# Kernel tuning notes

Hardware: AMD Instinct MI355X
Metric: run time of the kernel (lower is better)

Reference implementation:

```python
import math
import jax, jax.numpy as jnp
import numpy as np
from jax import lax

CELL = 8
BINS = 9


def setup_inputs() -> dict:
    key = jax.random.key(0)
    x = jax.random.uniform(key, (64, 3, 224, 224), dtype=jnp.float32)
    return {"x": x}


def reference(x):
    N, C, H, W = x.shape
    # Fixed Sobel buffers: one output channel summing over all input channels.
    sob = jnp.array([[-1.0, 0.0, 1.0], [-2.0, 0.0, 2.0], [-1.0, 0.0, 1.0]], dtype=x.dtype)
    kx = jnp.broadcast_to(sob, (1, C, 3, 3))          # SobelX weight [O=1, I=C, 3, 3]
    ky = jnp.broadcast_to(sob.T, (1, C, 3, 3))        # SobelY weight
    dn = ('NCHW', 'OIHW', 'NCHW')
    gx = lax.conv_general_dilated(x, kx, (1, 1), 'SAME', dimension_numbers=dn)  # [N,1,H,W]
    gy = lax.conv_general_dilated(x, ky, (1, 1), 'SAME', dimension_numbers=dn)
    mag = jnp.sqrt(gx * gx + gy * gy)                 # [N,1,H,W]
    ang = jnp.abs(jnp.arctan2(gx, gy))                # unsigned gradients -> [0, pi]
    bin_idx = jnp.floor(ang / math.pi * (BINS - 1)).astype(jnp.int32)  # [N,1,H,W], values in [0, BINS-1]
    # scatter_(1, bin_idx, mag) == one-hot along bin axis times magnitude
    onehot = (bin_idx == jnp.arange(BINS, dtype=jnp.int32)[None, :, None, None]).astype(x.dtype)  # [N,BINS,H,W]
    vol = onehot * mag                                # broadcast over bin axis
    # AvgPool2d(cell) * cell^2 == per-cell sum
    hog = vol.reshape(N, BINS, H // CELL, CELL, W // CELL, CELL).sum(axis=(3, 5))  # [N,BINS,H/8,W/8]
    return hog.reshape(N, -1)
```

## Files before the change

### kernel.cpp

```cpp
#include <hip/hip_runtime.h>
#include <math.h>


namespace {
constexpr int Himg = 224;
constexpr int Wimg = 224;
constexpr int NCELL = 28;
constexpr int BINS  = 9;
constexpr int ROWS  = 18;
constexpr int LDSW  = 232;
constexpr int NCHUNK = ROWS * 56;

__global__ __launch_bounds__(512) void hog_kernel(const float* __restrict__ x,
                                                  float* __restrict__ out) {
    const int n  = blockIdx.y;
    const int pr = blockIdx.x;
    const int t  = threadIdx.x;

    __shared__ float s[ROWS][LDSW];
    __shared__ float h2[448 * BINS];

    if (t < ROWS * 8) {
        int r = t >> 3;
        int c = t & 7;
        int col = (c < 4) ? c : (224 + c);
        s[r][col] = 0.0f;
    }

    const int h0 = pr * 16 - 1;
    const float* xb = x + (size_t)n * 3 * Himg * Wimg;

    float4 va[2];
    int    lofs[2];
    bool   act[2];
#pragma unroll
    for (int k = 0; k < 2; ++k) {
        int idx = t + 512 * k;
        bool pred = idx < NCHUNK;
        int r = pred ? (idx / 56) : 0;
        int q = idx - r * 56;
        int w = q * 4;
        int h = h0 + r;
        act[k]  = pred;
        lofs[k] = r * LDSW + 4 + w;
        float4 v = make_float4(0.f, 0.f, 0.f, 0.f);
        if (pred && h >= 0 && h < Himg) {
            const float* r0 = xb + (size_t)h * Wimg + w;
            float4 a = *(const float4*)(r0);
            float4 b = *(const float4*)(r0 + Himg * Wimg);
            float4 c4 = *(const float4*)(r0 + 2 * Himg * Wimg);
            v.x = a.x + b.x + c4.x;
            v.y = a.y + b.y + c4.y;
            v.z = a.z + b.z + c4.z;
            v.w = a.w + b.w + c4.w;
        }
        va[k] = v;
    }
#pragma unroll
    for (int k = 0; k < 2; ++k)
        if (act[k]) *(float4*)&((float*)s)[lofs[k]] = va[k];
    __syncthreads();

    const float PI_F = 3.14159265358979323846f;
    const float CK[8] = {0.92387953f, 0.70710678f, 0.38268343f, 0.0f,
                         -0.38268343f, -0.70710678f, -0.92387953f, -1.0f};

    if (t < 448) {
        const int g = t >> 5 >= 7 ? 1 : 0;
        const int gg = t / 224;
        const int w  = t - gg * 224;
        (void)g;
        const int rb = gg * 8;
        float ml = s[rb][3 + w], mc = s[rb][4 + w], mr = s[rb][5 + w];
        float zl = s[rb + 1][3 + w], zc = s[rb + 1][4 + w], zr = s[rb + 1][5 + w];
        float acc[BINS];
#pragma unroll
        for (int j = 0; j < BINS; ++j) acc[j] = 0.0f;

#pragma unroll
        for (int i = 0; i < 8; ++i) {
            float pl = s[rb + i + 2][3 + w];
            float pc = s[rb + i + 2][4 + w];
            float pr2 = s[rb + i + 2][5 + w];

            float gx = (mr - ml) + 2.0f * (zr - zl) + (pr2 - pl);
            float gy = (pl + 2.0f * pc + pr2) - (ml + 2.0f * mc + mr);
            float mag = sqrtf(gx * gx + gy * gy);

            float negy = -gy;
            int bin = 0;
            float guard = 1e30f;
#pragma unroll
            for (int j = 0; j < 8; ++j) {
                float sj = fmaf(mag, CK[j], negy);
                bin += (sj >= 0.0f) ? 1 : 0;
                guard = fminf(guard, fabsf(sj));
            }
            if (guard < mag * 1e-4f) {
                float ang = fabsf(atan2f(gx, gy));
                bin = (int)(ang / PI_F * 8.0f);
                bin = bin > 8 ? 8 : bin;
            }
#pragma unroll
            for (int j = 0; j < BINS; ++j) acc[j] += (bin == j) ? mag : 0.0f;

            ml = zl; mc = zc; mr = zr;
            zl = pl; zc = pc; zr = pr2;
        }
#pragma unroll
        for (int j = 0; j < BINS; ++j) h2[t * BINS + j] = acc[j];
    }
    __syncthreads();

    if (t < 2 * NCELL * BINS) {
        int grp = t / (NCELL * BINS);
        int rem = t - grp * (NCELL * BINS);
        int bin = rem / NCELL;
        int cw  = rem - bin * NCELL;
        int cr  = pr * 2 + grp;
        float v = 0.0f;
#pragma unroll
        for (int c = 0; c < 8; ++c)
            v += h2[(grp * 224 + cw * 8 + c) * BINS + bin];
        out[((size_t)n * BINS + bin) * (NCELL * NCELL) + (size_t)cr * NCELL + cw] = v;
    }
}
}

extern "C" void kernel_launch(void* const* d_in, const int* in_sizes, int n_in,
                              void* d_out, int out_size, void* d_ws, size_t ws_size,
                              hipStream_t stream) {
    const float* x = (const float*)d_in[0];
    float* out = (float*)d_out;
    const int N = in_sizes[0] / (3 * Himg * Wimg);
    dim3 grid(NCELL / 2, N);
    hog_kernel<<<grid, 512, 0, stream>>>(x, out);
}
```

Before: 83.50 us.

## Process one cell row per block and reduce cell histograms with shuffles

Each block now covers a single 8-row cell band with 256 threads instead of two bands with 512, doubling the grid. The shared-memory histogram buffer and its extra barrier are replaced by in-wavefront shuffle reductions over 8 adjacent columns. This cuts LDS use and synchronization to raise occupancy, at the cost of a larger halo fraction (10 rows loaded per 8 computed) and more redundant global reads.

```diff
diff --git a/kernel.cpp b/kernel.cpp
--- a/kernel.cpp
+++ b/kernel.cpp
@@ -7,18 +7,17 @@
 constexpr int Wimg = 224;
 constexpr int NCELL = 28;
 constexpr int BINS  = 9;
-constexpr int ROWS  = 18;
+constexpr int ROWS  = 10;
 constexpr int LDSW  = 232;
 constexpr int NCHUNK = ROWS * 56;
 
-__global__ __launch_bounds__(512) void hog_kernel(const float* __restrict__ x,
-                                                  float* __restrict__ out) {
+__global__ __launch_bounds__(256, 6) void hog_kernel(const float* __restrict__ x,
+                                                     float* __restrict__ out) {
     const int n  = blockIdx.y;
-    const int pr = blockIdx.x;
+    const int cr = blockIdx.x;
     const int t  = threadIdx.x;
 
     __shared__ float s[ROWS][LDSW];
-    __shared__ float h2[448 * BINS];
 
     if (t < ROWS * 8) {
         int r = t >> 3;
@@ -27,16 +26,16 @@
         s[r][col] = 0.0f;
     }
 
-    const int h0 = pr * 16 - 1;
+    const int h0 = cr * 8 - 1;
     const float* xb = x + (size_t)n * 3 * Himg * Wimg;
 
-    float4 va[2];
-    int    lofs[2];
-    bool   act[2];
+    float4 va[3];
+    int    lofs[3];
+    bool   act[3];
 #pragma unroll
-    for (int k = 0; k < 2; ++k) {
-        int idx = t + 512 * k;
-        bool pred = idx < NCHUNK;
+    for (int k = 0; k < 3; ++k) {
+        int idx = t + 256 * k;
+        bool pred = (k < 2) || (idx < NCHUNK);
         int r = pred ? (idx / 56) : 0;
         int q = idx - r * 56;
         int w = q * 4;
@@ -46,8 +45,8 @@
         float4 v = make_float4(0.f, 0.f, 0.f, 0.f);
         if (pred && h >= 0 && h < Himg) {
             const float* r0 = xb + (size_t)h * Wimg + w;
-            float4 a = *(const float4*)(r0);
-            float4 b = *(const float4*)(r0 + Himg * Wimg);
+            float4 a  = *(const float4*)(r0);
+            float4 b  = *(const float4*)(r0 + Himg * Wimg);
             float4 c4 = *(const float4*)(r0 + 2 * Himg * Wimg);
             v.x = a.x + b.x + c4.x;
             v.y = a.y + b.y + c4.y;
@@ -57,7 +56,7 @@
         va[k] = v;
     }
 #pragma unroll
-    for (int k = 0; k < 2; ++k)
+    for (int k = 0; k < 3; ++k)
         if (act[k]) *(float4*)&((float*)s)[lofs[k]] = va[k];
     __syncthreads();
 
@@ -65,26 +64,22 @@
     const float CK[8] = {0.92387953f, 0.70710678f, 0.38268343f, 0.0f,
                          -0.38268343f, -0.70710678f, -0.92387953f, -1.0f};
 
-    if (t < 448) {
-        const int g = t >> 5 >= 7 ? 1 : 0;
-        const int gg = t / 224;
-        const int w  = t - gg * 224;
-        (void)g;
-        const int rb = gg * 8;
-        float ml = s[rb][3 + w], mc = s[rb][4 + w], mr = s[rb][5 + w];
-        float zl = s[rb + 1][3 + w], zc = s[rb + 1][4 + w], zr = s[rb + 1][5 + w];
+    if (t < 224) {
+        const int w = t;
+        float ml = s[0][3 + w], mc = s[0][4 + w], mr = s[0][5 + w];
+        float zl = s[1][3 + w], zc = s[1][4 + w], zr = s[1][5 + w];
         float acc[BINS];
 #pragma unroll
         for (int j = 0; j < BINS; ++j) acc[j] = 0.0f;
 
 #pragma unroll
         for (int i = 0; i < 8; ++i) {
-            float pl = s[rb + i + 2][3 + w];
-            float pc = s[rb + i + 2][4 + w];
-            float pr2 = s[rb + i + 2][5 + w];
+            float pl = s[i + 2][3 + w];
+            float pc = s[i + 2][4 + w];
+            float pr = s[i + 2][5 + w];
 
-            float gx = (mr - ml) + 2.0f * (zr - zl) + (pr2 - pl);
-            float gy = (pl + 2.0f * pc + pr2) - (ml + 2.0f * mc + mr);
+            float gx = (mr - ml) + 2.0f * (zr - zl) + (pr - pl);
+            float gy = (pl + 2.0f * pc + pr) - (ml + 2.0f * mc + mr);
             float mag = sqrtf(gx * gx + gy * gy);
 
             float negy = -gy;
@@ -105,24 +100,23 @@
             for (int j = 0; j < BINS; ++j) acc[j] += (bin == j) ? mag : 0.0f;
 
             ml = zl; mc = zc; mr = zr;
-            zl = pl; zc = pc; zr = pr2;
+            zl = pl; zc = pc; zr = pr;
         }
+
 #pragma unroll
-        for (int j = 0; j < BINS; ++j) h2[t * BINS + j] = acc[j];
-    }
-    __syncthreads();
-
-    if (t < 2 * NCELL * BINS) {
-        int grp = t / (NCELL * BINS);
-        int rem = t - grp * (NCELL * BINS);
-        int bin = rem / NCELL;
-        int cw  = rem - bin * NCELL;
-        int cr  = pr * 2 + grp;
-        float v = 0.0f;
+        for (int j = 0; j < BINS; ++j) {
+            float v = acc[j];
+            v += __shfl_down(v, 4);
+            v += __shfl_down(v, 2);
+            v += __shfl_down(v, 1);
+            acc[j] = v;
+        }
+        if ((w & 7) == 0) {
+            const int cw = w >> 3;
 #pragma unroll
-        for (int c = 0; c < 8; ++c)
-            v += h2[(grp * 224 + cw * 8 + c) * BINS + bin];
-        out[((size_t)n * BINS + bin) * (NCELL * NCELL) + (size_t)cr * NCELL + cw] = v;
+            for (int j = 0; j < BINS; ++j)
+                out[((size_t)n * BINS + j) * (NCELL * NCELL) + (size_t)cr * NCELL + cw] = acc[j];
+        }
     }
 }
 }
@@ -133,6 +127,6 @@
     const float* x = (const float*)d_in[0];
     float* out = (float*)d_out;
     const int N = in_sizes[0] / (3 * Himg * Wimg);
-    dim3 grid(NCELL / 2, N);
-    hog_kernel<<<grid, 512, 0, stream>>>(x, out);
+    dim3 grid(NCELL, N);
+    hog_kernel<<<grid, 256, 0, stream>>>(x, out);
 }
```

Measured after the change: 83.89 us. No clear change (+0.5%).
